# Kernel optimization log

Hardware: AMD Instinct MI355X
Metric: run time of the kernel (lower is better)

The kernel has to match this reference:

```python
import jax, jax.numpy as jnp
import numpy as np

SEQ, BATCH, D_MODEL = 128, 64, 2048
D_STATE, D_CONV, CHUNK = 16, 4, 32
D_INNER = int(1.2 * D_MODEL)      # 2457
GROUPS = 7                        # largest g<=8 dividing 2457
DT_RANK = max(4, D_MODEL // 64)   # 32
WIN = 8
NEG = -1e30


def setup_inputs() -> dict:
    key = jax.random.key(0)
    ks = jax.random.split(key, 8)
    w = lambda k, shape, s: (jax.random.normal(k, shape) * s).astype(jnp.float32)
    return {
        "x": jax.random.normal(ks[0], (SEQ, BATCH, D_MODEL), dtype=jnp.float32),
        "W_in": w(ks[1], (D_INNER, D_MODEL), 0.02),
        "b_in": jnp.zeros((D_INNER,), jnp.float32),
        "W_gate": w(ks[2], (D_INNER, D_MODEL), 0.02),
        "b_gate": jnp.zeros((D_INNER,), jnp.float32),
        "W_conv": w(ks[3], (D_INNER, D_INNER // GROUPS, D_CONV), 0.05),
        "b_conv": jnp.zeros((D_INNER,), jnp.float32),
        "W_xproj": w(ks[4], (DT_RANK + D_STATE, D_INNER), 0.02),
        "b_xproj": jnp.zeros((DT_RANK + D_STATE,), jnp.float32),
        "W_dt": w(ks[5], (D_INNER, DT_RANK), 0.1),
        "Dparam": jnp.full((D_INNER,), 0.1, jnp.float32),
        "W_out": w(ks[6], (D_MODEL, D_INNER), 0.02),
        "b_out": jnp.zeros((D_MODEL,), jnp.float32),
        "ln_w": jnp.ones((D_MODEL,), jnp.float32),
        "ln_b": jnp.zeros((D_MODEL,), jnp.float32),
    }


def reference(x, W_in, b_in, W_gate, b_gate, W_conv, b_conv,
              W_xproj, b_xproj, W_dt, Dparam, W_out, b_out, ln_w, ln_b):
    def process_chunk(xc_in):                      # [L, B, d_model]
        L = xc_in.shape[0]
        xi = xc_in @ W_in.T + b_in                 # [L, B, d_inner]
        z = xc_in @ W_gate.T + b_gate              # gate
        # causal grouped conv1d: torch pads both sides by d_conv-1 then
        # truncates [:L]  ==  left-pad (d_conv-1), VALID conv
        c = jnp.transpose(xi, (1, 2, 0))           # [B, d_inner, L]
        c = jnp.pad(c, ((0, 0), (0, 0), (D_CONV - 1, 0)))
        c = jax.lax.conv_general_dilated(
            c, W_conv, window_strides=(1,), padding='VALID',
            dimension_numbers=('NCH', 'OIH', 'NCH'),
            feature_group_count=GROUPS) + b_conv[None, :, None]
        xc = jax.nn.silu(jnp.transpose(c, (2, 0, 1)))   # [L, B, d_inner]
        # dt_t = softplus(dt_proj(x_proj(x_t)[:dt_rank])) + 1e-4
        xp = xc @ W_xproj.T + b_xproj
        dt = jax.nn.softplus(xp[..., :DT_RANK] @ W_dt.T) + 1e-4  # [L,B,d_inner]
        xpad = jnp.pad(xc, ((WIN - 1, 0), (0, 0), (0, 0)))
        windows = jnp.stack([xpad[k:k + L] for k in range(WIN)], axis=1)
        t = jnp.arange(L)
        kk = jnp.arange(WIN)
        offset = jnp.maximum(0, WIN - 1 - t)       # shift so arange starts at 0
        ar = kk[None, :] - offset[:, None]
        valid = ar >= 0
        logits = dt[:, None] * ar[:, :, None, None].astype(dt.dtype)
        logits = jnp.where(valid[:, :, None, None], logits, NEG)
        wgt = jax.nn.softmax(logits, axis=1)       # softmax over window
        local = jnp.sum(wgt * windows, axis=1)     # [L, B, d_inner]
        return (local + Dparam * xc) * jax.nn.sigmoid(z)

    # chunks are processed independently (window + conv restart per chunk)
    xr = x.reshape(SEQ // CHUNK, CHUNK, BATCH, D_MODEL)
    ys = jax.vmap(process_chunk)(xr).reshape(SEQ, BATCH, D_INNER)
    compressed = ys[-WIN:].mean(axis=0)            # mean of last 8 steps
    out = compressed @ W_out.T + b_out             # [B, d_model]
    mu = out.mean(-1, keepdims=True)
    var = ((out - mu) ** 2).mean(-1, keepdims=True)
    return ((out - mu) / jnp.sqrt(var + 1e-5)) * ln_w + ln_b
```

## Files before the change

kernel.cpp:

```cpp
#include <hip/hip_runtime.h>
#include <math.h>
#include <stdint.h>

#define DMODEL 2048
#define DINNER 2457
#define NI     2464
#define GROUPS 7
#define GCH    351
#define GP     352
#define GNP    384
#define NROW_XI 1152
#define NROW_Z  512
#define NCAT   5120
#define GATE0  2560
#define OUT_SPLITS 16
#define CONV_PLANE (GROUPS * GNP * GP)

typedef __attribute__((ext_vector_type(8))) __bf16 bf16x8;
typedef __attribute__((ext_vector_type(4))) float f32x4;
typedef __attribute__((ext_vector_type(8))) unsigned short ushort8;

__device__ inline unsigned short f2bf(float f) {
    union { float f; unsigned int u; } v; v.f = f;
    unsigned int u = v.u;
    return (unsigned short)((u + 0x7FFFu + ((u >> 16) & 1u)) >> 16);
}

__device__ inline int lds_addr(int row, int slot) {
    return row * 32 + ((slot ^ ((row >> 1) & 3)) << 3);
}

__device__ __forceinline__ void gload16(const unsigned short* g, unsigned short* l) {
    __builtin_amdgcn_global_load_lds(
        (const __attribute__((address_space(1))) unsigned int*)g,
        (__attribute__((address_space(3))) unsigned int*)l, 16, 0, 0);
}

#define CAST_B0 1152
#define CAST_B1 6066
#define CAST_B2 9435
__global__ __launch_bounds__(256)
void cast_all(const float* __restrict__ x110,
              const float* __restrict__ Win, const float* __restrict__ Wg,
              const float* __restrict__ Wc,
              unsigned short* __restrict__ A_x,
              unsigned short* __restrict__ B_cat,
              unsigned short* __restrict__ B_cv)
{
    int bx = blockIdx.x;
    if (bx < CAST_B0) {
        size_t t = (size_t)bx * 256 + threadIdx.x;
        const float4* s = (const float4*)x110 + t * 2;
        float4 a = s[0], b = s[1];
        ushort8 o;
        o[0]=f2bf(a.x); o[1]=f2bf(a.y); o[2]=f2bf(a.z); o[3]=f2bf(a.w);
        o[4]=f2bf(b.x); o[5]=f2bf(b.y); o[6]=f2bf(b.z); o[7]=f2bf(b.w);
        *(ushort8*)(A_x + t * 8) = o;
    } else if (bx < CAST_B1) {
        int idx = bx - CAST_B0;
        int half = idx >= DINNER;
        int cb = half ? idx - DINNER : idx;
        const float* src = half ? Wg : Win;
        size_t t = (size_t)cb * 256 + threadIdx.x;
        size_t elem = t * 8;
        size_t doff = elem + (half ? (size_t)GATE0 * DMODEL : 0);
        const float4* s = (const float4*)(src + elem);
        float4 a = s[0], b = s[1];
        ushort8 o;
        o[0]=f2bf(a.x); o[1]=f2bf(a.y); o[2]=f2bf(a.z); o[3]=f2bf(a.w);
        o[4]=f2bf(b.x); o[5]=f2bf(b.y); o[6]=f2bf(b.z); o[7]=f2bf(b.w);
        *(ushort8*)(B_cat + doff) = o;
    } else {
        int t = (bx - CAST_B1) * 256 + threadIdx.x;
        if (t >= DINNER * GCH) return;
        int oc = t / GCH, i = t - oc * GCH;
        float4 w = *(const float4*)(Wc + (size_t)t * 4);
        int g = oc / GCH, ol = oc - g * GCH;
        size_t base = (size_t)(g * GNP + ol) * GP + i;
        B_cv[0 * (size_t)CONV_PLANE + base] = f2bf(w.x);
        B_cv[1 * (size_t)CONV_PLANE + base] = f2bf(w.y);
        B_cv[2 * (size_t)CONV_PLANE + base] = f2bf(w.z);
        B_cv[3 * (size_t)CONV_PLANE + base] = f2bf(w.w);
        if (i == GCH - 1) {
            B_cv[0 * (size_t)CONV_PLANE + base + 1] = 0;
            B_cv[1 * (size_t)CONV_PLANE + base + 1] = 0;
            B_cv[2 * (size_t)CONV_PLANE + base + 1] = 0;
            B_cv[3 * (size_t)CONV_PLANE + base + 1] = 0;
        }
    }
}

#define NKF 64
__global__ __launch_bounds__(256)
void gemm_mfma_fused(const unsigned short* __restrict__ A,
                     const unsigned short* __restrict__ B,
                     const float* __restrict__ b_in,
                     const float* __restrict__ b_gate,
                     unsigned short* __restrict__ xi,
                     float* __restrict__ zb)
{
    __shared__ unsigned short sm[5 * 256 * 32];
    const int tid = threadIdx.x;
    const int w = tid >> 6, l = tid & 63;
    const int l15 = l & 15, l4 = l >> 4;
    const int wm = w >> 1, wn = w & 1;

    const int orig = blockIdx.x;
    const int xcd = orig & 7, lo = orig >> 3;
    const int logical = (xcd < 4 ? xcd * 33 : 132 + (xcd - 4) * 32) + lo;
    int mt, nt, is_gate;
    if (logical < 180) { nt = logical / 9; mt = logical % 9; is_gate = 0; }
    else { int b2 = logical - 180; nt = 20 + b2 / 4; mt = 5 + b2 % 4; is_gate = 1; }
    const int m0 = mt * 128, n0 = nt * 128;

    const int lr = l >> 2, slot = l & 3;
    const int r0 = w * 16 + lr, r1 = r0 + 64;
    const int xo0 = (slot ^ ((r0 >> 1) & 3)) << 3;
    const int xo1 = (slot ^ ((r1 >> 1) & 3)) << 3;
    const unsigned short* gA0 = A + (size_t)(m0 + r0) * DMODEL + xo0;
    const unsigned short* gA1 = A + (size_t)(m0 + r1) * DMODEL + xo1;
    const unsigned short* gB0 = B + (size_t)(n0 + r0) * DMODEL + xo0;
    const unsigned short* gB1 = B + (size_t)(n0 + r1) * DMODEL + xo1;
    unsigned short* dA0 = sm + w * 512;
    unsigned short* dA1 = sm + (w + 4) * 512;
    unsigned short* dB0 = sm + 4096 + w * 512;
    unsigned short* dB1 = sm + 4096 + (w + 4) * 512;

#define STAGE_G(buf, ks) do { int _o = (ks) * 32, _b = (buf) * 8192; \
    gload16(gA0 + _o, dA0 + _b); gload16(gA1 + _o, dA1 + _b); \
    gload16(gB0 + _o, dB0 + _b); gload16(gB1 + _o, dB1 + _b); } while (0)

    f32x4 acc[4][4] = {};
    auto compute = [&](const unsigned short* base) {
        bf16x8 af[4], bfr[4];
#pragma unroll
        for (int f = 0; f < 4; ++f)
            af[f] = *(const bf16x8*)(base + lds_addr(wm * 64 + f * 16 + l15, l4));
#pragma unroll
        for (int j = 0; j < 4; ++j)
            bfr[j] = *(const bf16x8*)(base + 4096 + lds_addr(wn * 64 + j * 16 + l15, l4));
        __builtin_amdgcn_s_setprio(1);
#pragma unroll
        for (int i = 0; i < 4; ++i)
#pragma unroll
            for (int j = 0; j < 4; ++j)
                acc[i][j] = __builtin_amdgcn_mfma_f32_16x16x32_bf16(af[i], bfr[j], acc[i][j], 0, 0, 0);
        __builtin_amdgcn_s_setprio(0);
    };

    STAGE_G(0, 0); STAGE_G(1, 1); STAGE_G(2, 2); STAGE_G(3, 3);
    int rbuf = 0, sbuf = 4;
    for (int ks = 0; ks < NKF - 4; ++ks) {
        asm volatile("s_waitcnt vmcnt(12)" ::: "memory");
        __builtin_amdgcn_s_barrier();
        STAGE_G(sbuf, ks + 4);
        compute(sm + rbuf * 8192);
        rbuf = rbuf == 4 ? 0 : rbuf + 1;
        sbuf = sbuf == 4 ? 0 : sbuf + 1;
    }
    asm volatile("s_waitcnt vmcnt(12)" ::: "memory");
    __builtin_amdgcn_s_barrier();
    compute(sm + rbuf * 8192); rbuf = rbuf == 4 ? 0 : rbuf + 1;
    asm volatile("s_waitcnt vmcnt(8)" ::: "memory");
    __builtin_amdgcn_s_barrier();
    compute(sm + rbuf * 8192); rbuf = rbuf == 4 ? 0 : rbuf + 1;
    asm volatile("s_waitcnt vmcnt(4)" ::: "memory");
    __builtin_amdgcn_s_barrier();
    compute(sm + rbuf * 8192); rbuf = rbuf == 4 ? 0 : rbuf + 1;
    asm volatile("s_waitcnt vmcnt(0)" ::: "memory");
    __builtin_amdgcn_s_barrier();
    compute(sm + rbuf * 8192);
#undef STAGE_G

    if (!is_gate) {
#pragma unroll
        for (int j = 0; j < 4; ++j) {
            int colg = n0 + wn * 64 + j * 16 + l15;
            if (colg < DINNER) {
                int g = colg / GCH, ci = colg - g * GCH;
                float bias = b_in[colg];
                size_t dco = (size_t)(g * GP + ci);
#pragma unroll
                for (int i = 0; i < 4; ++i)
#pragma unroll
                    for (int r = 0; r < 4; ++r) {
                        int row = m0 + wm * 64 + i * 16 + l4 * 4 + r;
                        xi[(size_t)row * NI + dco] = f2bf(acc[i][j][r] + bias);
                        if (ci == GCH - 1) xi[(size_t)row * NI + dco + 1] = 0;
                    }
            }
        }
    } else {
#pragma unroll
        for (int j = 0; j < 4; ++j) {
            int ng = n0 + wn * 64 + j * 16 + l15 - GATE0;
            if (ng < DINNER) {
                float bias = b_gate[ng];
#pragma unroll
                for (int i = 0; i < 4; ++i)
#pragma unroll
                    for (int r = 0; r < 4; ++r) {
                        int row = m0 + wm * 64 + i * 16 + l4 * 4 + r;
                        zb[(size_t)(row - 640) * NI + ng] = acc[i][j][r] + bias;
                    }
            }
        }
    }
}

#define NKC 44
__global__ __launch_bounds__(256)
void conv_mfma(const unsigned short* __restrict__ xi,
               const unsigned short* __restrict__ Bc,
               const float* __restrict__ bc,
               float* __restrict__ xcb)
{
    __shared__ unsigned short sm[5 * 192 * 32];
    const int tid = threadIdx.x;
    const int w = tid >> 6, l = tid & 63;
    const int l15 = l & 15, l4 = l >> 4;
    const int wm = w >> 1, wn = w & 1;

    const int orig = blockIdx.x;
    const int xcd = orig & 7, lo = orig >> 3;
    const int logical = (xcd < 3 ? xcd * 40 : 120 + (xcd - 3) * 39) + lo;
    const int gn = logical / 15, mt = logical % 15;
    const int g = gn / 3, nt = gn % 3;
    const int m0 = mt * 64;
    const int n0l = nt * 128;

    const int lr = l >> 2, slot = l & 3;
    const int rA = w * 16 + lr;
    const int rB1 = rA + 64;
    const int xoA  = (slot ^ ((rA  >> 1) & 3)) << 3;
    const int xoB1 = (slot ^ ((rB1 >> 1) & 3)) << 3;
    const unsigned short* gAb = xi + (size_t)(m0 + rA) * NI + g * GP + xoA;
    const unsigned short* gB0 = Bc + (size_t)(g * GNP + n0l + rA) * GP + xoA;
    const unsigned short* gB1 = Bc + (size_t)(g * GNP + n0l + rB1) * GP + xoB1;
    unsigned short* dA  = sm + w * 512;
    unsigned short* dB0 = sm + 2048 + w * 512;
    unsigned short* dB1 = sm + 2048 + (w + 4) * 512;

#define STAGE_C(buf, ks) do { \
    int _tap = (ks) / 11, _kc = (ks) - _tap * 11, _b = (buf) * 6144; \
    size_t _ao = (size_t)(64 * _tap) * NI + _kc * 32; \
    size_t _bo = (size_t)_tap * CONV_PLANE + _kc * 32; \
    gload16(gAb + _ao, dA  + _b); \
    gload16(gB0 + _bo, dB0 + _b); \
    gload16(gB1 + _bo, dB1 + _b); } while (0)

    f32x4 acc[2][4] = {};
    auto compute = [&](const unsigned short* base) {
        bf16x8 af[2], bfr[4];
#pragma unroll
        for (int f = 0; f < 2; ++f)
            af[f] = *(const bf16x8*)(base + lds_addr(wm * 32 + f * 16 + l15, l4));
#pragma unroll
        for (int j = 0; j < 4; ++j)
            bfr[j] = *(const bf16x8*)(base + 2048 + lds_addr(wn * 64 + j * 16 + l15, l4));
        __builtin_amdgcn_s_setprio(1);
#pragma unroll
        for (int i = 0; i < 2; ++i)
#pragma unroll
            for (int j = 0; j < 4; ++j)
                acc[i][j] = __builtin_amdgcn_mfma_f32_16x16x32_bf16(af[i], bfr[j], acc[i][j], 0, 0, 0);
        __builtin_amdgcn_s_setprio(0);
    };

    STAGE_C(0, 0); STAGE_C(1, 1); STAGE_C(2, 2); STAGE_C(3, 3);
    int rbuf = 0, sbuf = 4;
    for (int ks = 0; ks < NKC - 4; ++ks) {
        asm volatile("s_waitcnt vmcnt(9)" ::: "memory");
        __builtin_amdgcn_s_barrier();
        STAGE_C(sbuf, ks + 4);
        compute(sm + rbuf * 6144);
        rbuf = rbuf == 4 ? 0 : rbuf + 1;
        sbuf = sbuf == 4 ? 0 : sbuf + 1;
    }
    asm volatile("s_waitcnt vmcnt(9)" ::: "memory");
    __builtin_amdgcn_s_barrier();
    compute(sm + rbuf * 6144); rbuf = rbuf == 4 ? 0 : rbuf + 1;
    asm volatile("s_waitcnt vmcnt(6)" ::: "memory");
    __builtin_amdgcn_s_barrier();
    compute(sm + rbuf * 6144); rbuf = rbuf == 4 ? 0 : rbuf + 1;
    asm volatile("s_waitcnt vmcnt(3)" ::: "memory");
    __builtin_amdgcn_s_barrier();
    compute(sm + rbuf * 6144); rbuf = rbuf == 4 ? 0 : rbuf + 1;
    asm volatile("s_waitcnt vmcnt(0)" ::: "memory");
    __builtin_amdgcn_s_barrier();
    compute(sm + rbuf * 6144);
#undef STAGE_C

#pragma unroll
    for (int j = 0; j < 4; ++j) {
        int ocl = n0l + wn * 64 + j * 16 + l15;
        if (ocl < GCH) {
            int ch = g * GCH + ocl;
            float bias = bc[ch];
#pragma unroll
            for (int i = 0; i < 2; ++i)
#pragma unroll
                for (int r = 0; r < 4; ++r) {
                    int row = m0 + wm * 32 + i * 16 + l4 * 4 + r;
                    float v = acc[i][j][r] + bias;
                    xcb[(size_t)row * NI + ch] = v / (1.f + expf(-v));
                }
        }
    }
}

__global__ __launch_bounds__(256)
void xproj_dt(const float* __restrict__ xc,
              const float* __restrict__ Wxp,
              const float* __restrict__ bxp,
              const float* __restrict__ Wdt,
              float* __restrict__ dtb)
{
    const int r0 = blockIdx.x * 4;
    const float* a = xc + (size_t)(448 + r0) * NI;
    float acc[4][32];
#pragma unroll
    for (int ri = 0; ri < 4; ++ri)
#pragma unroll
        for (int o = 0; o < 32; ++o) acc[ri][o] = 0.f;
    for (int k = threadIdx.x; k < DINNER; k += 256) {
        float av0 = a[k], av1 = a[NI + k], av2 = a[2 * NI + k], av3 = a[3 * NI + k];
#pragma unroll
        for (int o = 0; o < 32; ++o) {
            float wv = Wxp[(size_t)o * DINNER + k];
            acc[0][o] = fmaf(av0, wv, acc[0][o]);
            acc[1][o] = fmaf(av1, wv, acc[1][o]);
            acc[2][o] = fmaf(av2, wv, acc[2][o]);
            acc[3][o] = fmaf(av3, wv, acc[3][o]);
        }
    }
#pragma unroll
    for (int ri = 0; ri < 4; ++ri)
#pragma unroll
        for (int o = 0; o < 32; ++o)
#pragma unroll
            for (int off = 32; off; off >>= 1)
                acc[ri][o] += __shfl_down(acc[ri][o], off);
    __shared__ float red[4][4][32];
    __shared__ float xp[4][32];
    const int wid = threadIdx.x >> 6, lane = threadIdx.x & 63;
    if (lane == 0)
#pragma unroll
        for (int ri = 0; ri < 4; ++ri)
#pragma unroll
            for (int o = 0; o < 32; ++o) red[wid][ri][o] = acc[ri][o];
    __syncthreads();
    if (threadIdx.x < 128) {
        int ri = threadIdx.x >> 5, o = threadIdx.x & 31;
        xp[ri][o] = red[0][ri][o] + red[1][ri][o] + red[2][ri][o] + red[3][ri][o] + bxp[o];
    }
    __syncthreads();
    float xr[4][32];
#pragma unroll
    for (int ri = 0; ri < 4; ++ri)
#pragma unroll
        for (int k = 0; k < 32; ++k) xr[ri][k] = xp[ri][k];
    for (int o = threadIdx.x; o < DINNER; o += 256) {
        const float4* wp = (const float4*)(Wdt + (size_t)o * 32);
        float s0 = 0.f, s1 = 0.f, s2 = 0.f, s3 = 0.f;
#pragma unroll
        for (int q = 0; q < 8; ++q) {
            float4 wv = wp[q];
            s0 = fmaf(xr[0][q*4+0], wv.x, s0); s0 = fmaf(xr[0][q*4+1], wv.y, s0);
            s0 = fmaf(xr[0][q*4+2], wv.z, s0); s0 = fmaf(xr[0][q*4+3], wv.w, s0);
            s1 = fmaf(xr[1][q*4+0], wv.x, s1); s1 = fmaf(xr[1][q*4+1], wv.y, s1);
            s1 = fmaf(xr[1][q*4+2], wv.z, s1); s1 = fmaf(xr[1][q*4+3], wv.w, s1);
            s2 = fmaf(xr[2][q*4+0], wv.x, s2); s2 = fmaf(xr[2][q*4+1], wv.y, s2);
            s2 = fmaf(xr[2][q*4+2], wv.z, s2); s2 = fmaf(xr[2][q*4+3], wv.w, s2);
            s3 = fmaf(xr[3][q*4+0], wv.x, s3); s3 = fmaf(xr[3][q*4+1], wv.y, s3);
            s3 = fmaf(xr[3][q*4+2], wv.z, s3); s3 = fmaf(xr[3][q*4+3], wv.w, s3);
        }
        dtb[(size_t)(r0 + 0) * NI + o] = fmaxf(s0, 0.f) + log1pf(expf(-fabsf(s0))) + 1e-4f;
        dtb[(size_t)(r0 + 1) * NI + o] = fmaxf(s1, 0.f) + log1pf(expf(-fabsf(s1))) + 1e-4f;
        dtb[(size_t)(r0 + 2) * NI + o] = fmaxf(s2, 0.f) + log1pf(expf(-fabsf(s2))) + 1e-4f;
        dtb[(size_t)(r0 + 3) * NI + o] = fmaxf(s3, 0.f) + log1pf(expf(-fabsf(s3))) + 1e-4f;
    }
}

__global__ __launch_bounds__(256)
void fuse_kernel(const float* __restrict__ xc, const float* __restrict__ z,
                 const float* __restrict__ dt, const float* __restrict__ Dp,
                 float* __restrict__ comp)
{
    const int d = blockIdx.x * 256 + threadIdx.x;
    const int b = blockIdx.y;
    if (d >= DINNER) return;
    float xcv[15];
#pragma unroll
    for (int tt = 0; tt < 15; ++tt) xcv[tt] = xc[(size_t)(tt * 64 + b) * NI + d];
    const float Dpd = Dp[d];
    float acc = 0.f;
#pragma unroll
    for (int s = 0; s < 8; ++s) {
        float dval = dt[(size_t)(s * 64 + b) * NI + d];
        float zval = z[(size_t)(s * 64 + b) * NI + d];
        float e = expf(-dval);
        float w = 1.f, wsum = 0.f, lsum = 0.f;
#pragma unroll
        for (int k = 7; k >= 0; --k) {
            wsum += w;
            lsum = fmaf(w, xcv[s + k], lsum);
            w *= e;
        }
        float local = lsum / wsum;
        float ys = (local + Dpd * xcv[s + 7]) / (1.f + expf(-zval));
        acc += ys;
    }
    comp[(size_t)b * NI + d] = acc * 0.125f;
}

__global__ __launch_bounds__(256)
void gemm_nt_splitk(const float* __restrict__ A, int lda,
                    const float* __restrict__ B, int ldb,
                    float* __restrict__ Cp, int ldc,
                    int M, int N, int K, int kchunk)
{
    __shared__ float As[16][68];
    __shared__ float Bs[16][68];
    const int tid = threadIdx.x;
    const int tx = tid & 15, ty = tid >> 4;
    const int m0 = blockIdx.y * 64, n0 = blockIdx.x * 64;
    const int kbeg = blockIdx.z * kchunk;
    const int kend = min(K, kbeg + kchunk);
    float* C = Cp + (size_t)blockIdx.z * M * ldc;
    float acc[4][4] = {};
    for (int k0 = kbeg; k0 < kend; k0 += 16) {
#pragma unroll
        for (int u = 0; u < 4; ++u) {
            int idx = u * 256 + tid;
            int r = idx >> 4, kk = idx & 15;
            int gk = k0 + kk;
            float av = 0.f, bv = 0.f;
            if (gk < kend) {
                av = A[(size_t)(m0 + r) * lda + gk];
                int nn = n0 + r;
                bv = (nn < N) ? B[(size_t)nn * ldb + gk] : 0.f;
            }
            As[kk][r] = av;
            Bs[kk][r] = bv;
        }
        __syncthreads();
#pragma unroll
        for (int kk = 0; kk < 16; ++kk) {
            float4 a4 = *(const float4*)&As[kk][ty * 4];
            float4 b4 = *(const float4*)&Bs[kk][tx * 4];
            float a[4] = {a4.x, a4.y, a4.z, a4.w};
            float b[4] = {b4.x, b4.y, b4.z, b4.w};
#pragma unroll
            for (int i = 0; i < 4; ++i)
#pragma unroll
                for (int j = 0; j < 4; ++j)
                    acc[i][j] = fmaf(a[i], b[j], acc[i][j]);
        }
        __syncthreads();
    }
#pragma unroll
    for (int i = 0; i < 4; ++i) {
        int m = m0 + ty * 4 + i;
#pragma unroll
        for (int j = 0; j < 4; ++j) {
            int n = n0 + tx * 4 + j;
            if (n < N) C[(size_t)m * ldc + n] = acc[i][j];
        }
    }
}

__global__ __launch_bounds__(256)
void ln_kernel(const float* __restrict__ Cp,
               const float* __restrict__ b_out,
               const float* __restrict__ lw, const float* __restrict__ lb,
               float* __restrict__ out)
{
    const int b = blockIdx.x;
    const int tid = threadIdx.x;
    __shared__ float red[4];
    float v[8];
    float s = 0.f;
#pragma unroll
    for (int i = 0; i < 8; ++i) {
        int col = i * 256 + tid;
        float acc = b_out[col];
#pragma unroll
        for (int p = 0; p < OUT_SPLITS; ++p)
            acc += Cp[(size_t)p * 64 * 2048 + b * 2048 + col];
        v[i] = acc; s += acc;
    }
#pragma unroll
    for (int off = 32; off; off >>= 1) s += __shfl_down(s, off);
    if ((tid & 63) == 0) red[tid >> 6] = s;
    __syncthreads();
    float mu = (red[0] + red[1] + red[2] + red[3]) / 2048.f;
    float s2 = 0.f;
#pragma unroll
    for (int i = 0; i < 8; ++i) { float dd = v[i] - mu; s2 += dd * dd; }
#pragma unroll
    for (int off = 32; off; off >>= 1) s2 += __shfl_down(s2, off);
    __syncthreads();
    if ((tid & 63) == 0) red[tid >> 6] = s2;
    __syncthreads();
    float var = (red[0] + red[1] + red[2] + red[3]) / 2048.f;
    float inv = rsqrtf(var + 1e-5f);
#pragma unroll
    for (int i = 0; i < 8; ++i) {
        int dcol = i * 256 + tid;
        out[b * 2048 + dcol] = (v[i] - mu) * inv * lw[dcol] + lb[dcol];
    }
}

extern "C" void kernel_launch(void* const* d_in, const int* in_sizes, int n_in,
                              void* d_out, int out_size, void* d_ws, size_t ws_size,
                              hipStream_t stream)
{
    const float* x      = (const float*)d_in[0];
    const float* W_in   = (const float*)d_in[1];
    const float* b_in   = (const float*)d_in[2];
    const float* W_gate = (const float*)d_in[3];
    const float* b_gate = (const float*)d_in[4];
    const float* W_conv = (const float*)d_in[5];
    const float* b_conv = (const float*)d_in[6];
    const float* W_xp   = (const float*)d_in[7];
    const float* b_xp   = (const float*)d_in[8];
    const float* W_dt   = (const float*)d_in[9];
    const float* Dp     = (const float*)d_in[10];
    const float* W_out  = (const float*)d_in[11];
    const float* b_out  = (const float*)d_in[12];
    const float* ln_w   = (const float*)d_in[13];
    const float* ln_b   = (const float*)d_in[14];
    float* out = (float*)d_out;

    float* ws = (float*)d_ws;
    auto alloc = [&](size_t nf) { float* p = ws; ws += (nf + 255) & ~(size_t)255; return p; };
    unsigned short* A_x   = (unsigned short*)alloc((size_t)NROW_XI * DMODEL / 2);
    unsigned short* B_cat = (unsigned short*)alloc((size_t)NCAT * DMODEL / 2);
    unsigned short* B_cv  = (unsigned short*)alloc((size_t)4 * CONV_PLANE / 2);
    unsigned short* xi_bf = (unsigned short*)alloc((size_t)NROW_XI * NI / 2);
    float* zb   = alloc((size_t)NROW_Z * NI);
    float* comp = alloc((size_t)64 * NI);
    float* xcb     = (float*)B_cat;
    float* outpart = (float*)B_cat + (size_t)960 * NI;
    float* dtb     = (float*)B_cv;

    cast_all<<<CAST_B2, 256, 0, stream>>>(x + (size_t)(110 * 64) * DMODEL,
                                          W_in, W_gate, W_conv, A_x, B_cat, B_cv);
    gemm_mfma_fused<<<260, 256, 0, stream>>>(A_x, B_cat, b_in, b_gate, xi_bf, zb);
    conv_mfma<<<315, 256, 0, stream>>>(xi_bf, B_cv, b_conv, xcb);
    xproj_dt<<<128, 256, 0, stream>>>(xcb, W_xp, b_xp, W_dt, dtb);
    {
        dim3 grid((DINNER + 255) / 256, 64);
        fuse_kernel<<<grid, 256, 0, stream>>>(xcb, zb, dtb, Dp, comp);
    }
    {
        const int kchunk = (DINNER + OUT_SPLITS - 1) / OUT_SPLITS;
        dim3 grid(DMODEL / 64, 1, OUT_SPLITS);
        gemm_nt_splitk<<<grid, 256, 0, stream>>>(comp, NI, W_out, DINNER,
                                                 outpart, DMODEL, 64, DMODEL, DINNER, kchunk);
    }
    ln_kernel<<<64, 256, 0, stream>>>(outpart, b_out, ln_w, ln_b, out);
}
```

Measured before the change: 140.7 us.

## Fuse dt projection and softplus into fuse kernel, shrink xproj to per-row kernel

Splits the old xproj_dt kernel. A new xp_kernel computes only the 32-wide x_proj outputs, one block per row (512 blocks instead of 128), and writes a small buffer. The dt_proj matvec and softplus move into fuse_kernel, which loads the per-channel W_dt row into registers and recomputes dt on the fly. This avoids writing and re-reading the full 512x2464 dt buffer and improves parallelism of the x_proj reduction. In exchange it adds register pressure and recomputes W_dt dot products in each of the 64 batch blocks.

```diff
diff --git a/kernel.cpp b/kernel.cpp
--- a/kernel.cpp
+++ b/kernel.cpp
@@ -310,86 +310,65 @@
 }
 
 __global__ __launch_bounds__(256)
-void xproj_dt(const float* __restrict__ xc,
-              const float* __restrict__ Wxp,
-              const float* __restrict__ bxp,
-              const float* __restrict__ Wdt,
-              float* __restrict__ dtb)
-{
-    const int r0 = blockIdx.x * 4;
-    const float* a = xc + (size_t)(448 + r0) * NI;
-    float acc[4][32];
-#pragma unroll
-    for (int ri = 0; ri < 4; ++ri)
-#pragma unroll
-        for (int o = 0; o < 32; ++o) acc[ri][o] = 0.f;
+void xp_kernel(const float* __restrict__ xc,
+               const float* __restrict__ Wxp,
+               const float* __restrict__ bxp,
+               float* __restrict__ xp32)
+{
+    const int row = blockIdx.x;
+    const float* a = xc + (size_t)(448 + row) * NI;
+    float acc[32];
+#pragma unroll
+    for (int o = 0; o < 32; ++o) acc[o] = 0.f;
     for (int k = threadIdx.x; k < DINNER; k += 256) {
-        float av0 = a[k], av1 = a[NI + k], av2 = a[2 * NI + k], av3 = a[3 * NI + k];
-#pragma unroll
-        for (int o = 0; o < 32; ++o) {
-            float wv = Wxp[(size_t)o * DINNER + k];
-            acc[0][o] = fmaf(av0, wv, acc[0][o]);
-            acc[1][o] = fmaf(av1, wv, acc[1][o]);
-            acc[2][o] = fmaf(av2, wv, acc[2][o]);
-            acc[3][o] = fmaf(av3, wv, acc[3][o]);
-        }
-    }
-#pragma unroll
-    for (int ri = 0; ri < 4; ++ri)
+        float av = a[k];
 #pragma unroll
         for (int o = 0; o < 32; ++o)
-#pragma unroll
-            for (int off = 32; off; off >>= 1)
-                acc[ri][o] += __shfl_down(acc[ri][o], off);
-    __shared__ float red[4][4][32];
-    __shared__ float xp[4][32];
+            acc[o] = fmaf(av, Wxp[(size_t)o * DINNER + k], acc[o]);
+    }
+#pragma unroll
+    for (int o = 0; o < 32; ++o)
+#pragma unroll
+        for (int off = 32; off; off >>= 1)
+            acc[o] += __shfl_down(acc[o], off);
+    __shared__ float red[4][32];
     const int wid = threadIdx.x >> 6, lane = threadIdx.x & 63;
     if (lane == 0)
 #pragma unroll
-        for (int ri = 0; ri < 4; ++ri)
-#pragma unroll
-            for (int o = 0; o < 32; ++o) red[wid][ri][o] = acc[ri][o];
+        for (int o = 0; o < 32; ++o) red[wid][o] = acc[o];
     __syncthreads();
-    if (threadIdx.x < 128) {
-        int ri = threadIdx.x >> 5, o = threadIdx.x & 31;
-        xp[ri][o] = red[0][ri][o] + red[1][ri][o] + red[2][ri][o] + red[3][ri][o] + bxp[o];
-    }
-    __syncthreads();
-    float xr[4][32];
-#pragma unroll
-    for (int ri = 0; ri < 4; ++ri)
-#pragma unroll
-        for (int k = 0; k < 32; ++k) xr[ri][k] = xp[ri][k];
-    for (int o = threadIdx.x; o < DINNER; o += 256) {
-        const float4* wp = (const float4*)(Wdt + (size_t)o * 32);
-        float s0 = 0.f, s1 = 0.f, s2 = 0.f, s3 = 0.f;
-#pragma unroll
-        for (int q = 0; q < 8; ++q) {
-            float4 wv = wp[q];
-            s0 = fmaf(xr[0][q*4+0], wv.x, s0); s0 = fmaf(xr[0][q*4+1], wv.y, s0);
-            s0 = fmaf(xr[0][q*4+2], wv.z, s0); s0 = fmaf(xr[0][q*4+3], wv.w, s0);
-            s1 = fmaf(xr[1][q*4+0], wv.x, s1); s1 = fmaf(xr[1][q*4+1], wv.y, s1);
-            s1 = fmaf(xr[1][q*4+2], wv.z, s1); s1 = fmaf(xr[1][q*4+3], wv.w, s1);
-            s2 = fmaf(xr[2][q*4+0], wv.x, s2); s2 = fmaf(xr[2][q*4+1], wv.y, s2);
-            s2 = fmaf(xr[2][q*4+2], wv.z, s2); s2 = fmaf(xr[2][q*4+3], wv.w, s2);
-            s3 = fmaf(xr[3][q*4+0], wv.x, s3); s3 = fmaf(xr[3][q*4+1], wv.y, s3);
-            s3 = fmaf(xr[3][q*4+2], wv.z, s3); s3 = fmaf(xr[3][q*4+3], wv.w, s3);
-        }
-        dtb[(size_t)(r0 + 0) * NI + o] = fmaxf(s0, 0.f) + log1pf(expf(-fabsf(s0))) + 1e-4f;
-        dtb[(size_t)(r0 + 1) * NI + o] = fmaxf(s1, 0.f) + log1pf(expf(-fabsf(s1))) + 1e-4f;
-        dtb[(size_t)(r0 + 2) * NI + o] = fmaxf(s2, 0.f) + log1pf(expf(-fabsf(s2))) + 1e-4f;
-        dtb[(size_t)(r0 + 3) * NI + o] = fmaxf(s3, 0.f) + log1pf(expf(-fabsf(s3))) + 1e-4f;
+    if (threadIdx.x < 32) {
+        int o = threadIdx.x;
+        xp32[row * 32 + o] = red[0][o] + red[1][o] + red[2][o] + red[3][o] + bxp[o];
     }
 }
 
 __global__ __launch_bounds__(256)
 void fuse_kernel(const float* __restrict__ xc, const float* __restrict__ z,
-                 const float* __restrict__ dt, const float* __restrict__ Dp,
+                 const float* __restrict__ xp,
+                 const float* __restrict__ Wdt,
+                 const float* __restrict__ Dp,
                  float* __restrict__ comp)
 {
     const int d = blockIdx.x * 256 + threadIdx.x;
     const int b = blockIdx.y;
+    __shared__ float xps[8][32];
+    {
+        int s = threadIdx.x >> 5, o = threadIdx.x & 31;
+        xps[s][o] = xp[((s * 64) + b) * 32 + o];
+    }
+    __syncthreads();
     if (d >= DINNER) return;
+    float wd[32];
+    {
+        const float4* wp = (const float4*)(Wdt + (size_t)d * 32);
+#pragma unroll
+        for (int q = 0; q < 8; ++q) {
+            float4 v = wp[q];
+            wd[q * 4 + 0] = v.x; wd[q * 4 + 1] = v.y;
+            wd[q * 4 + 2] = v.z; wd[q * 4 + 3] = v.w;
+        }
+    }
     float xcv[15];
 #pragma unroll
     for (int tt = 0; tt < 15; ++tt) xcv[tt] = xc[(size_t)(tt * 64 + b) * NI + d];
@@ -397,7 +376,10 @@
     float acc = 0.f;
 #pragma unroll
     for (int s = 0; s < 8; ++s) {
-        float dval = dt[(size_t)(s * 64 + b) * NI + d];
+        float sv = 0.f;
+#pragma unroll
+        for (int k = 0; k < 32; ++k) sv = fmaf(xps[s][k], wd[k], sv);
+        float dval = fmaxf(sv, 0.f) + log1pf(expf(-fabsf(sv))) + 1e-4f;
         float zval = z[(size_t)(s * 64 + b) * NI + d];
         float e = expf(-dval);
         float w = 1.f, wsum = 0.f, lsum = 0.f;
@@ -540,19 +522,19 @@
     unsigned short* B_cv  = (unsigned short*)alloc((size_t)4 * CONV_PLANE / 2);
     unsigned short* xi_bf = (unsigned short*)alloc((size_t)NROW_XI * NI / 2);
     float* zb   = alloc((size_t)NROW_Z * NI);
+    float* xp32 = alloc((size_t)512 * 32);
     float* comp = alloc((size_t)64 * NI);
     float* xcb     = (float*)B_cat;
     float* outpart = (float*)B_cat + (size_t)960 * NI;
-    float* dtb     = (float*)B_cv;
 
     cast_all<<<CAST_B2, 256, 0, stream>>>(x + (size_t)(110 * 64) * DMODEL,
                                           W_in, W_gate, W_conv, A_x, B_cat, B_cv);
     gemm_mfma_fused<<<260, 256, 0, stream>>>(A_x, B_cat, b_in, b_gate, xi_bf, zb);
     conv_mfma<<<315, 256, 0, stream>>>(xi_bf, B_cv, b_conv, xcb);
-    xproj_dt<<<128, 256, 0, stream>>>(xcb, W_xp, b_xp, W_dt, dtb);
+    xp_kernel<<<512, 256, 0, stream>>>(xcb, W_xp, b_xp, xp32);
     {
         dim3 grid((DINNER + 255) / 256, 64);
-        fuse_kernel<<<grid, 256, 0, stream>>>(xcb, zb, dtb, Dp, comp);
+        fuse_kernel<<<grid, 256, 0, stream>>>(xcb, zb, xp32, W_dt, Dp, comp);
     }
     {
         const int kchunk = (DINNER + OUT_SPLITS - 1) / OUT_SPLITS;
```

Result: faster. 126.8 us (-9.9%).
